# Performance work log

Hardware: AMD Instinct MI355X
Metric: run time of the kernel (lower is better)

## Reference

```python
import jax, jax.numpy as jnp
import numpy as np

B, S, D = 4, 2048, 1024
H = 16
HD = D // H  # 64


def setup_inputs() -> dict:
    key = jax.random.key(0)
    ks = jax.random.split(key, 9)
    sc = 1.0 / np.sqrt(D)
    return {
        "hidden_states": jax.random.normal(ks[0], (B, S, D), jnp.float32),
        "Wq": jax.random.normal(ks[1], (D, D), jnp.float32) * sc,
        "bq": jnp.zeros((D,), jnp.float32),
        "Wk": jax.random.normal(ks[2], (D, D), jnp.float32) * sc,
        "bk": jnp.zeros((D,), jnp.float32),
        "Wv": jax.random.normal(ks[3], (D, D), jnp.float32) * sc,
        "bv": jnp.zeros((D,), jnp.float32),
        "Wo": jax.random.normal(ks[4], (D, D), jnp.float32) * sc,
        "bo": jnp.zeros((D,), jnp.float32),
    }


def _rope_emb(seq_len, head_dim, dtype):
    # Faithful to torch buffer: emb = cat(sin(pos*inv_freq), cos(pos*inv_freq))
    inv_freq = 1.0 / (10000.0 ** (jnp.arange(0, head_dim, 2, dtype=jnp.float32) / head_dim))
    sinusoid = jnp.arange(seq_len, dtype=jnp.float32)[:, None] * inv_freq[None, :]  # [S, hd/2]
    return jnp.concatenate([jnp.sin(sinusoid), jnp.cos(sinusoid)], axis=-1).astype(dtype)  # [S, hd]


def _rotate(x, c, s):
    # x: [B,H,S,hd]; c,s: [1,1,S,hd/2]
    x1, x2 = x[..., : HD // 2], x[..., HD // 2 :]
    return jnp.concatenate([x1 * c - x2 * s, x2 * c + x1 * s], axis=-1)


def reference(hidden_states, Wq, bq, Wk, bk, Wv, bv, Wo, bo):
    b, s, d = hidden_states.shape

    def proj(W, bias):
        y = jnp.einsum("bsd,ed->bse", hidden_states, W) + bias
        return y.reshape(b, s, H, HD).transpose(0, 2, 1, 3)  # [B,H,S,hd]

    q, k, v = proj(Wq, bq), proj(Wk, bk), proj(Wv, bv)

    emb = _rope_emb(s, HD, hidden_states.dtype)
    # NOTE: original code names first half 'cos' though the buffer stores sin first.
    c = emb[None, None, :, : HD // 2]
    sn = emb[None, None, :, HD // 2 :]
    q = _rotate(q, c, sn)
    k = _rotate(k, c, sn)

    scores = jnp.einsum("bhqd,bhkd->bhqk", q, k) / jnp.sqrt(jnp.asarray(HD, hidden_states.dtype))
    probs = jax.nn.softmax(scores, axis=-1)
    ctx = jnp.einsum("bhqk,bhkd->bhqd", probs, v)
    ctx = ctx.transpose(0, 2, 1, 3).reshape(b, s, d)  # [B,S,D]
    return jnp.einsum("bsd,ed->bse", ctx, Wo) + bo
```

## Files before the change

kernel.cpp:

```cpp
#include <hip/hip_runtime.h>
#include <cmath>

#define B_ 4
#define S_ 2048
#define D_ 1024
#define H_ 16
#define HD_ 64

typedef __attribute__((ext_vector_type(8))) _Float16 half8;
typedef __attribute__((ext_vector_type(2))) _Float16 half2t;
typedef __attribute__((ext_vector_type(2))) __fp16 fp16x2;
typedef __attribute__((ext_vector_type(4))) float floatx4;
typedef __attribute__((ext_vector_type(16))) float floatx16;
typedef __attribute__((ext_vector_type(2))) unsigned uint2v;

typedef const __attribute__((address_space(1))) uint4 gbl_uint4;
typedef __attribute__((address_space(3))) uint4 lds_uint4;

union H2U { unsigned u; half2t h; fp16x2 f; };
__device__ __forceinline__ unsigned hpack2(float a, float b) {
    H2U x; x.h[0] = (_Float16)a; x.h[1] = (_Float16)b; return x.u;
}
__device__ __forceinline__ unsigned pkrtz(float a, float b) {
    H2U x; x.f = __builtin_amdgcn_cvt_pkrtz(a, b); return x.u;
}
__device__ __forceinline__ float h_lo(unsigned u) { H2U x; x.u = u; return (float)x.h[0]; }
__device__ __forceinline__ float h_hi(unsigned u) { H2U x; x.u = u; return (float)x.h[1]; }

__device__ __forceinline__ void barrier_lgkm() {
    asm volatile("s_waitcnt lgkmcnt(0)\n\ts_barrier" ::: "memory");
}

__global__ __launch_bounds__(256)
void conv_x(const float* __restrict__ x, unsigned short* __restrict__ o, int n)
{
    const int i = (blockIdx.x * 256 + threadIdx.x) * 8;
    if (i >= n) return;
    const float4 a = *(const float4*)(x + i);
    const float4 b = *(const float4*)(x + i + 4);
    *(uint4*)(o + i) = make_uint4(hpack2(a.x, a.y), hpack2(a.z, a.w),
                                  hpack2(b.x, b.y), hpack2(b.z, b.w));
}

__global__ __launch_bounds__(256)
void conv_weights(const float* __restrict__ Wq, const float* __restrict__ Wk,
                  const float* __restrict__ Wv, const float* __restrict__ Wo,
                  const float* __restrict__ bq, const float* __restrict__ bk,
                  const float* __restrict__ bv,
                  unsigned short* __restrict__ Wqkvf, unsigned short* __restrict__ Wof,
                  float* __restrict__ bqkv)
{
    const int bxx = blockIdx.x;
    const int t = threadIdx.x;
    if (bxx < 2048) {
        const int w = bxx >> 9;
        const int i = ((bxx & 511) * 256 + t) * 8;
        const float* src = (w == 0) ? Wq : (w == 1) ? Wk : (w == 2) ? Wv : Wo;
        const float4 a = *(const float4*)(src + i);
        const float4 b = *(const float4*)(src + i + 4);
        const uint4 v = make_uint4(hpack2(a.x, a.y), hpack2(a.z, a.w),
                                   hpack2(b.x, b.y), hpack2(b.z, b.w));
        if (w < 3)
            *(uint4*)(Wqkvf + (size_t)w * 1048576 + i) = v;
        else
            *(uint4*)(Wof + i) = v;
    } else {
        const int idx = t * 4;
        *(float4*)(bqkv + idx)        = *(const float4*)(bq + idx);
        *(float4*)(bqkv + 1024 + idx) = *(const float4*)(bk + idx);
        *(float4*)(bqkv + 2048 + idx) = *(const float4*)(bv + idx);
    }
}

template<int OBF>
__global__ __launch_bounds__(256)
void gemm_half(const unsigned short* __restrict__ Ap, const unsigned short* __restrict__ Bp,
               const float* __restrict__ bias, void* __restrict__ Cout,
               int M, int N, int K)
{
    __shared__ uint4 ASH[2][512];
    __shared__ uint4 BSH[2][512];

    const int tid = threadIdx.x;
    const int bm = blockIdx.x * 128;
    const int bn = blockIdx.y * 128;
    const int w = tid >> 6, l = tid & 63;
    const int wm = (w & 1) * 64, wn = (w >> 1) * 64;

    floatx4 acc[4][4];
#pragma unroll
    for (int i = 0; i < 4; ++i)
#pragma unroll
        for (int j = 0; j < 4; ++j)
#pragma unroll
            for (int r = 0; r < 4; ++r) acc[i][j][r] = 0.f;

    const size_t gA0 = (size_t)(bm + (2 * w) * 16 + (l & 15)) * K + (l >> 4) * 8;
    const size_t gA1 = gA0 + (size_t)16 * K;
    const size_t gB0 = (size_t)(bn + (2 * w) * 16 + (l & 15)) * K + (l >> 4) * 8;
    const size_t gB1 = gB0 + (size_t)16 * K;

    const int am = (wm >> 4) * 64 + l;
    const int bnf = (wn >> 4) * 64 + l;

    __builtin_amdgcn_global_load_lds((gbl_uint4*)(Ap + gA0), (lds_uint4*)&ASH[0][w * 128],      16, 0, 0);
    __builtin_amdgcn_global_load_lds((gbl_uint4*)(Ap + gA1), (lds_uint4*)&ASH[0][w * 128 + 64], 16, 0, 0);
    __builtin_amdgcn_global_load_lds((gbl_uint4*)(Bp + gB0), (lds_uint4*)&BSH[0][w * 128],      16, 0, 0);
    __builtin_amdgcn_global_load_lds((gbl_uint4*)(Bp + gB1), (lds_uint4*)&BSH[0][w * 128 + 64], 16, 0, 0);

    for (int k0 = 0; k0 < K; k0 += 32) {
        const int cur = (k0 >> 5) & 1;
        __syncthreads();
        if (k0 + 32 < K) {
            const int nxt = cur ^ 1;
            const int kn = k0 + 32;
            __builtin_amdgcn_global_load_lds((gbl_uint4*)(Ap + gA0 + kn), (lds_uint4*)&ASH[nxt][w * 128],      16, 0, 0);
            __builtin_amdgcn_global_load_lds((gbl_uint4*)(Ap + gA1 + kn), (lds_uint4*)&ASH[nxt][w * 128 + 64], 16, 0, 0);
            __builtin_amdgcn_global_load_lds((gbl_uint4*)(Bp + gB0 + kn), (lds_uint4*)&BSH[nxt][w * 128],      16, 0, 0);
            __builtin_amdgcn_global_load_lds((gbl_uint4*)(Bp + gB1 + kn), (lds_uint4*)&BSH[nxt][w * 128 + 64], 16, 0, 0);
        }

        const half8* pA = (const half8*)ASH[cur];
        const half8* pB = (const half8*)BSH[cur];

        half8 a[4];
#pragma unroll
        for (int i = 0; i < 4; ++i) a[i] = pA[am + i * 64];
#pragma unroll
        for (int j = 0; j < 4; ++j) {
            const half8 b = pB[bnf + j * 64];
#pragma unroll
            for (int i = 0; i < 4; ++i)
                acc[i][j] = __builtin_amdgcn_mfma_f32_16x16x32_f16(a[i], b, acc[i][j], 0, 0, 0);
        }
    }

    const int cr = (l >> 4) << 2;
    const int cc = l & 15;
#pragma unroll
    for (int j = 0; j < 4; ++j) {
        const int col = bn + wn + j * 16 + cc;
        const float bv = bias[col];
#pragma unroll
        for (int i = 0; i < 4; ++i) {
            const int row = bm + wm + i * 16 + cr;
#pragma unroll
            for (int r = 0; r < 4; ++r) {
                const float vv = acc[i][j][r] + bv;
                if (OBF) {
                    ((unsigned short*)Cout)[(size_t)(row + r) * N + col] =
                        (unsigned short)(hpack2(vv, vv) & 0xffffu);
                } else {
                    ((float*)Cout)[(size_t)(row + r) * N + col] = vv;
                }
            }
        }
    }
}

__global__ __launch_bounds__(256)
void prep_fused(const unsigned short* __restrict__ qkv,
                unsigned short* __restrict__ Qf, unsigned short* __restrict__ Kfo,
                unsigned short* __restrict__ Vt)
{
    __shared__ unsigned T[64][65];
    const int bx = blockIdx.x;
    const int t = threadIdx.x;
    if (bx < B_ * S_) {
        const int s = bx & (S_ - 1);
        const size_t rbase = (size_t)bx * 3072;
        const size_t obase = (size_t)bx * D_;
        const int h = t >> 4;
        const int i2 = (t & 15) * 2;
        const float kfreq = 0.28782313662425572f;
        const float KS = 0.18033688011112042f;

        const float f0 = expf(-(float)i2 * kfreq);
        const float f1 = expf(-(float)(i2 + 1) * kfreq);
        const float t0 = (float)s * f0, t1 = (float)s * f1;
        const float sn0 = sinf(t0), cs0 = cosf(t0);
        const float sn1 = sinf(t1), cs1 = cosf(t1);

        const size_t c1 = (size_t)h * 64 + i2;
        const size_t c2 = c1 + 32;

        const unsigned uq1 = *(const unsigned*)(qkv + rbase + c1);
        const unsigned uq2 = *(const unsigned*)(qkv + rbase + c2);
        const unsigned uk1 = *(const unsigned*)(qkv + rbase + 1024 + c1);
        const unsigned uk2 = *(const unsigned*)(qkv + rbase + 1024 + c2);
        const float q1x = h_lo(uq1), q1y = h_hi(uq1);
        const float q2x = h_lo(uq2), q2y = h_hi(uq2);
        const float k1x = h_lo(uk1), k1y = h_hi(uk1);
        const float k2x = h_lo(uk2), k2y = h_hi(uk2);

        *(unsigned*)(Qf + obase + c1) = hpack2(q1x * sn0 - q2x * cs0, q1y * sn1 - q2y * cs1);
        *(unsigned*)(Qf + obase + c2) = hpack2(q2x * sn0 + q1x * cs0, q2y * sn1 + q1y * cs1);
        *(unsigned*)(Kfo + obase + c1) = hpack2((k1x * sn0 - k2x * cs0) * KS, (k1y * sn1 - k2y * cs1) * KS);
        *(unsigned*)(Kfo + obase + c2) = hpack2((k2x * sn0 + k1x * cs0) * KS, (k2y * sn1 + k1y * cs1) * KS);
    } else {
        const int vb = bx - B_ * S_;
        const int st = vb & 31;
        const int h  = (vb >> 5) & 15;
        const int b  = vb >> 9;
        const int s0 = st * 64;
#pragma unroll
        for (int it = 0; it < 2; ++it) {
            const int idx = it * 256 + t;
            const int row = idx >> 3;
            const int c8 = (idx & 7) * 8;
            const uint4 u = *(const uint4*)(qkv + ((size_t)(b * S_ + s0 + row)) * 3072 + 2048 + h * 64 + c8);
            T[row][c8+0] = u.x & 0xffffu; T[row][c8+1] = u.x >> 16;
            T[row][c8+2] = u.y & 0xffffu; T[row][c8+3] = u.y >> 16;
            T[row][c8+4] = u.z & 0xffffu; T[row][c8+5] = u.z >> 16;
            T[row][c8+6] = u.w & 0xffffu; T[row][c8+7] = u.w >> 16;
        }
        __syncthreads();
        const int d = t >> 2;
        const int scg = (t & 3) * 16;
        unsigned u[8];
#pragma unroll
        for (int ii = 0; ii < 8; ++ii)
            u[ii] = T[scg + 2*ii][d] | (T[scg + 2*ii + 1][d] << 16);
        unsigned short* dst = Vt + ((size_t)((b * H_ + h) * 64 + d)) * S_ + s0 + scg;
        *(uint4*)(dst)     = make_uint4(u[0], u[1], u[2], u[3]);
        *(uint4*)(dst + 8) = make_uint4(u[4], u[5], u[6], u[7]);
    }
}

__global__ __launch_bounds__(256)
void attn_mfma32(const unsigned short* __restrict__ Qf,
                 const unsigned short* __restrict__ Kfi,
                 const unsigned short* __restrict__ Vt,
                 unsigned short* __restrict__ Cf)
{
    __shared__ uint4 KF[2][512];
    __shared__ uint4 VF[2][512];

    const int t = threadIdx.x;
    const int i = blockIdx.x;
    const int xcd = i & 7, j = i >> 3;
    const int bh = xcd * 8 + (j >> 4);
    const int qblk = j & 15;
    const int b = bh >> 4, h = bh & 15;

    const int w = t >> 6, l = t & 63;
    const int lq = l & 31, h5 = l >> 5;
    const int qrow = qblk * 128 + w * 32 + lq;

    half8 qf[4];
    const unsigned short* qp = Qf + ((size_t)(b * S_ + qrow)) * D_ + h * 64 + h5 * 8;
#pragma unroll
    for (int kc = 0; kc < 4; ++kc) qf[kc] = *(const half8*)(qp + kc * 16);

    floatx16 o0, o1, o2, z16;
#pragma unroll
    for (int r = 0; r < 16; ++r) { o0[r] = 0.f; o1[r] = 0.f; o2[r] = 0.f; z16[r] = 0.f; }

    union { unsigned u[4]; half8 s; } onesf;
    const unsigned ov = (lq == 0) ? 0x3C003C00u : 0u;
    onesf.u[0] = ov; onesf.u[1] = ov; onesf.u[2] = ov; onesf.u[3] = ov;

    const int sr = t >> 2, sc = t & 3;
    const unsigned short* gK0 = Kfi + ((size_t)(b * S_ + sr)) * D_ + h * 64 + sc * 16;
    const unsigned short* gV0 = Vt + ((size_t)((b * H_ + h) * 64 + sr)) * S_ + sc * 16;
    const int e0 = (sr >> 5) * 256 + sc * 64 + ((sr & 31) ^ (sc << 1));
    const int lx[4] = { l, l ^ 2, l ^ 4, l ^ 6 };

    uint4 ka  = *(const uint4*)(gK0);
    uint4 kb2 = *(const uint4*)(gK0 + 8);
    uint4 va  = *(const uint4*)(gV0);
    uint4 vb2 = *(const uint4*)(gV0 + 8);
    KF[0][e0] = ka; KF[0][e0 + 32] = kb2;
    VF[0][e0] = va; VF[0][e0 + 32] = vb2;
    {
        const unsigned short* gK = gK0 + (size_t)64 * D_;
        const unsigned short* gV = gV0 + 64;
        ka  = *(const uint4*)(gK);
        kb2 = *(const uint4*)(gK + 8);
        va  = *(const uint4*)(gV);
        vb2 = *(const uint4*)(gV + 8);
    }
    __syncthreads();

    for (int kt = 0; kt < 32; ++kt) {
        const int cur = kt & 1;

        if (kt < 31) {
            uint4* wK = KF[cur ^ 1];
            uint4* wV = VF[cur ^ 1];
            wK[e0] = ka; wK[e0 + 32] = kb2;
            wV[e0] = va; wV[e0 + 32] = vb2;
        }
        if (kt < 30) {
            const unsigned short* gK = gK0 + (size_t)(kt + 2) * 64 * D_;
            const unsigned short* gV = gV0 + (size_t)(kt + 2) * 64;
            ka  = *(const uint4*)(gK);
            kb2 = *(const uint4*)(gK + 8);
            va  = *(const uint4*)(gV);
            vb2 = *(const uint4*)(gV + 8);
        }

        const half8* pKc = (const half8*)KF[cur];
        const half8* pVc = (const half8*)VF[cur];

        __builtin_amdgcn_s_setprio(1);
        floatx16 st0 = __builtin_amdgcn_mfma_f32_32x32x16_f16(pKc[lx[0]],           qf[0], z16, 0, 0, 0);
        floatx16 st1 = __builtin_amdgcn_mfma_f32_32x32x16_f16(pKc[4 * 64 + lx[0]],  qf[0], z16, 0, 0, 0);
#pragma unroll
        for (int kc = 1; kc < 4; ++kc) {
            st0 = __builtin_amdgcn_mfma_f32_32x32x16_f16(pKc[kc * 64 + lx[kc]],       qf[kc], st0, 0, 0, 0);
            st1 = __builtin_amdgcn_mfma_f32_32x32x16_f16(pKc[(4 + kc) * 64 + lx[kc]], qf[kc], st1, 0, 0, 0);
        }
        __builtin_amdgcn_s_setprio(0);

        unsigned pu0[8], pu1[8];
#pragma unroll
        for (int g = 0; g < 8; ++g) {
            pu0[g] = pkrtz(__builtin_amdgcn_exp2f(st0[2 * g]),
                           __builtin_amdgcn_exp2f(st0[2 * g + 1]));
            pu1[g] = pkrtz(__builtin_amdgcn_exp2f(st1[2 * g]),
                           __builtin_amdgcn_exp2f(st1[2 * g + 1]));
        }

        __builtin_amdgcn_s_setprio(1);
#pragma unroll
        for (int kc = 0; kc < 4; ++kc) {
            const unsigned* pus = (kc >> 1) ? pu1 : pu0;
            const int g0 = (kc & 1) * 4;
            const uint2v r02 = __builtin_amdgcn_permlane32_swap(pus[g0 + 0], pus[g0 + 2], false, false);
            const uint2v r13 = __builtin_amdgcn_permlane32_swap(pus[g0 + 1], pus[g0 + 3], false, false);
            union { unsigned u[4]; half8 s; } pf;
            pf.u[0] = r02[0];
            pf.u[1] = r13[0];
            pf.u[2] = r02[1];
            pf.u[3] = r13[1];
            o0 = __builtin_amdgcn_mfma_f32_32x32x16_f16(pVc[kc * 64 + lx[kc]],       pf.s, o0, 0, 0, 0);
            o1 = __builtin_amdgcn_mfma_f32_32x32x16_f16(pVc[(4 + kc) * 64 + lx[kc]], pf.s, o1, 0, 0, 0);
            o2 = __builtin_amdgcn_mfma_f32_32x32x16_f16(onesf.s,                     pf.s, o2, 0, 0, 0);
        }
        __builtin_amdgcn_s_setprio(0);

        if (kt < 31) barrier_lgkm();
    }

    union { float f; unsigned u; } lc; lc.f = o2[0];
    const uint2v lr = __builtin_amdgcn_permlane32_swap(lc.u, lc.u, false, false);
    union { unsigned u; float f; } ls; ls.u = lr[0];
    const float inv = 1.0f / ls.f;

    const size_t cbase = ((size_t)(b * S_ + qrow)) * D_ + h * 64;
#pragma unroll
    for (int rq = 0; rq < 4; ++rq) {
        const int d0 = rq * 8 + h5 * 4;
        const uint2 y0 = make_uint2(hpack2(o0[4*rq+0] * inv, o0[4*rq+1] * inv),
                                    hpack2(o0[4*rq+2] * inv, o0[4*rq+3] * inv));
        const uint2 y1 = make_uint2(hpack2(o1[4*rq+0] * inv, o1[4*rq+1] * inv),
                                    hpack2(o1[4*rq+2] * inv, o1[4*rq+3] * inv));
        *(uint2*)(Cf + cbase + d0)      = y0;
        *(uint2*)(Cf + cbase + 32 + d0) = y1;
    }
}

extern "C" void kernel_launch(void* const* d_in, const int* in_sizes, int n_in,
                              void* d_out, int out_size, void* d_ws, size_t ws_size,
                              hipStream_t stream) {
    (void)in_sizes; (void)n_in; (void)out_size; (void)ws_size;
    const float* X  = (const float*)d_in[0];
    const float* Wq = (const float*)d_in[1];
    const float* bq = (const float*)d_in[2];
    const float* Wk = (const float*)d_in[3];
    const float* bk = (const float*)d_in[4];
    const float* Wv = (const float*)d_in[5];
    const float* bv = (const float*)d_in[6];
    const float* Wo = (const float*)d_in[7];
    const float* bo = (const float*)d_in[8];
    float* out = (float*)d_out;

    char* ws = (char*)d_ws;
#define OFF(mb) (ws + ((size_t)(mb) << 20))
    unsigned short* Xf    = (unsigned short*)OFF(0);
    unsigned short* qkv16 = (unsigned short*)OFF(16);
    unsigned short* Qf    = (unsigned short*)OFF(64);
    unsigned short* Kfb   = (unsigned short*)OFF(80);
    unsigned short* Vtb   = (unsigned short*)OFF(96);
    unsigned short* Wqkvf = (unsigned short*)OFF(112);
    unsigned short* Wof   = (unsigned short*)OFF(118);
    float*          bqkv  = (float*)OFF(120);
    unsigned short* Cf    = (unsigned short*)OFF(0);
#undef OFF

    const int NX = B_ * S_ * D_;
    conv_x<<<NX / 2048, 256, 0, stream>>>(X, Xf, NX);
    conv_weights<<<2049, 256, 0, stream>>>(Wq, Wk, Wv, Wo, bq, bk, bv,
                                           Wqkvf, Wof, bqkv);
    gemm_half<1><<<dim3(64, 24), 256, 0, stream>>>(Xf, Wqkvf, bqkv,
                                                   qkv16, B_*S_, 3 * D_, D_);
    prep_fused<<<B_*S_ + 2048, 256, 0, stream>>>(qkv16, Qf, Kfb, Vtb);
    attn_mfma32<<<1024, 256, 0, stream>>>(Qf, Kfb, Vtb, Cf);
    gemm_half<0><<<dim3(64, 8), 256, 0, stream>>>(Cf, Wof, bo, out, B_*S_, D_, D_);
}
```

Before: 348.9 us.

## Triple-buffer GEMM LDS tiles with explicit vmcnt waits for deeper prefetch

```diff
diff --git a/kernel.cpp b/kernel.cpp
--- a/kernel.cpp
+++ b/kernel.cpp
@@ -78,8 +78,8 @@
                const float* __restrict__ bias, void* __restrict__ Cout,
                int M, int N, int K)
 {
-    __shared__ uint4 ASH[2][512];
-    __shared__ uint4 BSH[2][512];
+    __shared__ uint4 ASH[3][512];
+    __shared__ uint4 BSH[3][512];
 
     const int tid = threadIdx.x;
     const int bm = blockIdx.x * 128;
@@ -103,25 +103,32 @@
     const int am = (wm >> 4) * 64 + l;
     const int bnf = (wn >> 4) * 64 + l;
 
-    __builtin_amdgcn_global_load_lds((gbl_uint4*)(Ap + gA0), (lds_uint4*)&ASH[0][w * 128],      16, 0, 0);
-    __builtin_amdgcn_global_load_lds((gbl_uint4*)(Ap + gA1), (lds_uint4*)&ASH[0][w * 128 + 64], 16, 0, 0);
-    __builtin_amdgcn_global_load_lds((gbl_uint4*)(Bp + gB0), (lds_uint4*)&BSH[0][w * 128],      16, 0, 0);
-    __builtin_amdgcn_global_load_lds((gbl_uint4*)(Bp + gB1), (lds_uint4*)&BSH[0][w * 128 + 64], 16, 0, 0);
-
+    auto issue_tile = [&](int kn, int buf) {
+        __builtin_amdgcn_global_load_lds((gbl_uint4*)(Ap + gA0 + kn), (lds_uint4*)&ASH[buf][w * 128],      16, 0, 0);
+        __builtin_amdgcn_global_load_lds((gbl_uint4*)(Ap + gA1 + kn), (lds_uint4*)&ASH[buf][w * 128 + 64], 16, 0, 0);
+        __builtin_amdgcn_global_load_lds((gbl_uint4*)(Bp + gB0 + kn), (lds_uint4*)&BSH[buf][w * 128],      16, 0, 0);
+        __builtin_amdgcn_global_load_lds((gbl_uint4*)(Bp + gB1 + kn), (lds_uint4*)&BSH[buf][w * 128 + 64], 16, 0, 0);
+    };
+
+    issue_tile(0, 0);
+    if (32 < K) issue_tile(32, 1);
+
+    int buf = 0;
     for (int k0 = 0; k0 < K; k0 += 32) {
-        const int cur = (k0 >> 5) & 1;
-        __syncthreads();
         if (k0 + 32 < K) {
-            const int nxt = cur ^ 1;
-            const int kn = k0 + 32;
-            __builtin_amdgcn_global_load_lds((gbl_uint4*)(Ap + gA0 + kn), (lds_uint4*)&ASH[nxt][w * 128],      16, 0, 0);
-            __builtin_amdgcn_global_load_lds((gbl_uint4*)(Ap + gA1 + kn), (lds_uint4*)&ASH[nxt][w * 128 + 64], 16, 0, 0);
-            __builtin_amdgcn_global_load_lds((gbl_uint4*)(Bp + gB0 + kn), (lds_uint4*)&BSH[nxt][w * 128],      16, 0, 0);
-            __builtin_amdgcn_global_load_lds((gbl_uint4*)(Bp + gB1 + kn), (lds_uint4*)&BSH[nxt][w * 128 + 64], 16, 0, 0);
-        }
-
-        const half8* pA = (const half8*)ASH[cur];
-        const half8* pB = (const half8*)BSH[cur];
+            asm volatile("s_waitcnt vmcnt(4) lgkmcnt(0)" ::: "memory");
+        } else {
+            asm volatile("s_waitcnt vmcnt(0) lgkmcnt(0)" ::: "memory");
+        }
+        __builtin_amdgcn_s_barrier();
+
+        if (k0 + 64 < K) {
+            int nb = buf + 2; if (nb >= 3) nb -= 3;
+            issue_tile(k0 + 64, nb);
+        }
+
+        const half8* pA = (const half8*)ASH[buf];
+        const half8* pB = (const half8*)BSH[buf];
 
         half8 a[4];
 #pragma unroll
@@ -133,6 +140,8 @@
             for (int i = 0; i < 4; ++i)
                 acc[i][j] = __builtin_amdgcn_mfma_f32_16x16x32_f16(a[i], b, acc[i][j], 0, 0, 0);
         }
+
+        buf = (buf + 1 == 3) ? 0 : buf + 1;
     }
 
     const int cr = (l >> 4) << 2;
```

New measurement: 347.2 us. About the same (-0.5%).
